# Kernel optimization log

Hardware: AMD Instinct MI355X
Metric: run time of the kernel (lower is better)

The kernel has to match this reference:

```python
import jax, jax.numpy as jnp
import numpy as np

EMBED = 768
HEADS = 12
HEAD_DIM = EMBED // HEADS
HIDDEN = 4 * EMBED
EPS = 1e-5


def setup_inputs() -> dict:
    key = jax.random.key(0)
    ks = jax.random.split(key, 12)
    s = lambda fan_in: 1.0 / np.sqrt(fan_in)
    return {
        "x": jax.random.normal(ks[0], (4, 2048, EMBED), dtype=jnp.float32),
        "ln1_g": jnp.ones((EMBED,), jnp.float32),
        "ln1_b": jnp.zeros((EMBED,), jnp.float32),
        "qkv_w": jax.random.normal(ks[1], (EMBED, 3 * EMBED), jnp.float32) * s(EMBED),
        "qkv_b": jnp.zeros((3 * EMBED,), jnp.float32),
        "proj_w": jax.random.normal(ks[2], (EMBED, EMBED), jnp.float32) * s(EMBED),
        "proj_b": jnp.zeros((EMBED,), jnp.float32),
        "ln2_g": jnp.ones((EMBED,), jnp.float32),
        "ln2_b": jnp.zeros((EMBED,), jnp.float32),
        "fc1_w": jax.random.normal(ks[3], (EMBED, HIDDEN), jnp.float32) * s(EMBED),
        "fc1_b": jnp.zeros((HIDDEN,), jnp.float32),
        "fc2_w": jax.random.normal(ks[4], (HIDDEN, EMBED), jnp.float32) * s(HIDDEN),
        "fc2_b": jnp.zeros((EMBED,), jnp.float32),
    }


def _layernorm(x, g, b):
    mu = jnp.mean(x, axis=-1, keepdims=True)
    var = jnp.var(x, axis=-1, keepdims=True)
    return (x - mu) * jax.lax.rsqrt(var + EPS) * g + b


def reference(x, ln1_g, ln1_b, qkv_w, qkv_b, proj_w, proj_b,
              ln2_g, ln2_b, fc1_w, fc1_b, fc2_w, fc2_b):
    B, N, C = x.shape
    # --- attention (pre-LN) ---
    xn = _layernorm(x, ln1_g, ln1_b)
    qkv = xn @ qkv_w + qkv_b                       # [B,N,3C]
    qkv = qkv.reshape(B, N, 3, HEADS, HEAD_DIM)
    q, k, v = jnp.moveaxis(qkv, 2, 0)              # each [B,N,H,D]
    q = jnp.swapaxes(q, 1, 2)                      # [B,H,N,D]
    k = jnp.swapaxes(k, 1, 2)
    v = jnp.swapaxes(v, 1, 2)
    scale = HEAD_DIM ** -0.5
    attn = jax.nn.softmax(jnp.einsum('bhnd,bhmd->bhnm', q, k) * scale, axis=-1)
    out = jnp.einsum('bhnm,bhmd->bhnd', attn, v)   # [B,H,N,D]
    out = jnp.swapaxes(out, 1, 2).reshape(B, N, C)
    out = out @ proj_w + proj_b
    x = x + out
    # --- MLP (pre-LN) ---
    xn2 = _layernorm(x, ln2_g, ln2_b)
    h = jax.nn.gelu(xn2 @ fc1_w + fc1_b, approximate=False)
    x = x + (h @ fc2_w + fc2_b)
    return x
```

## Files before the change

kernel.cpp:

```cpp
#include <hip/hip_runtime.h>

typedef unsigned short ushort_t;
typedef __attribute__((ext_vector_type(8))) unsigned short ushort8;
typedef __attribute__((ext_vector_type(4))) unsigned short ushort4v;
typedef __attribute__((ext_vector_type(2))) unsigned int uint2v;
typedef __attribute__((ext_vector_type(4))) float f32x4;
typedef __attribute__((ext_vector_type(8))) __bf16 bf16x8;

#define DEVFN static __device__ __forceinline__

DEVFN unsigned short f2bf(float f) {
    unsigned int u = __builtin_bit_cast(unsigned int, f);
    u += 0x7FFFu + ((u >> 16) & 1u);
    return (unsigned short)(u >> 16);
}

DEVFN bf16x8 ldsfrag(const ushort_t* p) {
    ushort8 u = *reinterpret_cast<const ushort8*>(p);
    return __builtin_bit_cast(bf16x8, u);
}

DEVFN bf16x8 ldg8(const ushort_t* p) {
    ushort8 u = *reinterpret_cast<const ushort8*>(p);
    return __builtin_bit_cast(bf16x8, u);
}

DEVFN f32x4 mfma16(bf16x8 a, bf16x8 b, f32x4 c) {
    return __builtin_amdgcn_mfma_f32_16x16x32_bf16(a, b, c, 0, 0, 0);
}

DEVFN void gl2lds16(const ushort_t* g, ushort_t* l) {
    __builtin_amdgcn_global_load_lds(
        (const __attribute__((address_space(1))) unsigned int*)g,
        (__attribute__((address_space(3))) unsigned int*)l, 16, 0, 0);
}

DEVFN unsigned int cvtpk(float lo, float hi) {
    unsigned int r;
    asm("v_cvt_pk_bf16_f32 %0, %1, %2" : "=v"(r) : "v"(lo), "v"(hi));
    return r;
}

DEVFN float gelu_fast(float v) {
    const float a = 0.7978845608f * v * fmaf(0.044715f, v * v, 1.0f);
    const float e = __builtin_amdgcn_exp2f(2.885390082f * a);
    const float th = 1.0f - 2.0f * __builtin_amdgcn_rcpf(e + 1.0f);
    return 0.5f * v * (1.0f + th);
}

__global__ __launch_bounds__(256) void wt4_kernel(
    const float* __restrict__ qkv_w, const float* __restrict__ proj_w,
    const float* __restrict__ fc1_w, const float* __restrict__ fc2_w,
    ushort_t* __restrict__ qkv_wt, ushort_t* __restrict__ proj_wt,
    ushort_t* __restrict__ fc1_wt, ushort_t* __restrict__ fc2_wt) {
    __shared__ float t[32][33];
    const int bid = blockIdx.x;
    const float* in; ushort_t* out; int K, N, n0, k0;
    if (bid < 1728)      { in = qkv_w;  out = qkv_wt;  K = 768;  N = 2304;
                           n0 = (bid % 72) * 32;  k0 = (bid / 72) * 32; }
    else if (bid < 2304) { const int r = bid - 1728; in = proj_w; out = proj_wt;
                           K = 768;  N = 768;
                           n0 = (r % 24) * 32;    k0 = (r / 24) * 32; }
    else if (bid < 4608) { const int r = bid - 2304; in = fc1_w;  out = fc1_wt;
                           K = 768;  N = 3072;
                           n0 = (r % 96) * 32;    k0 = (r / 96) * 32; }
    else                 { const int r = bid - 4608; in = fc2_w;  out = fc2_wt;
                           K = 3072; N = 768;
                           n0 = (r % 24) * 32;    k0 = (r / 24) * 32; }
    const int tx = threadIdx.x & 31, ty = threadIdx.x >> 5;
    for (int j = 0; j < 4; j++)
        t[ty + 8 * j][tx] = in[(size_t)(k0 + ty + 8 * j) * N + n0 + tx];
    __syncthreads();
    for (int j = 0; j < 4; j++)
        out[(size_t)(n0 + ty + 8 * j) * K + k0 + tx] = f2bf(t[tx][ty + 8 * j]);
}

__global__ __launch_bounds__(256) void ln_kernel(const float* __restrict__ x,
                                                 const float* __restrict__ g,
                                                 const float* __restrict__ bta,
                                                 ushort_t* __restrict__ out) {
    const int row = blockIdx.x;
    const int tid = threadIdx.x;
    const float* xr = x + (size_t)row * 768;
    float v0 = xr[tid], v1 = xr[tid + 256], v2 = xr[tid + 512];
    float s = v0 + v1 + v2;
    float q = v0 * v0 + v1 * v1 + v2 * v2;
    for (int d = 32; d; d >>= 1) {
        s += __shfl_down(s, d);
        q += __shfl_down(q, d);
    }
    __shared__ float red[8];
    const int w = tid >> 6, lane = tid & 63;
    if (lane == 0) { red[w] = s; red[4 + w] = q; }
    __syncthreads();
    if (tid == 0) {
        float ts = red[0] + red[1] + red[2] + red[3];
        float tq = red[4] + red[5] + red[6] + red[7];
        float mu = ts * (1.0f / 768.0f);
        float var = tq * (1.0f / 768.0f) - mu * mu;
        red[0] = mu;
        red[1] = rsqrtf(var + 1e-5f);
    }
    __syncthreads();
    const float mu = red[0], rs = red[1];
    ushort_t* orow = out + (size_t)row * 768;
    orow[tid]       = f2bf((v0 - mu) * rs * g[tid]       + bta[tid]);
    orow[tid + 256] = f2bf((v1 - mu) * rs * g[tid + 256] + bta[tid + 256]);
    orow[tid + 512] = f2bf((v2 - mu) * rs * g[tid + 512] + bta[tid + 512]);
}

enum { EPI_QKV = 0, EPI_RES = 1, EPI_GELU = 2 };

template <int EPI, int BN, int BK>
__global__ __launch_bounds__(256) void gemm_kernel(
    const ushort_t* __restrict__ A, const ushort_t* __restrict__ BT,
    const float* __restrict__ bias, const float* __restrict__ resid,
    float* __restrict__ outf, ushort_t* __restrict__ outb,
    ushort_t* __restrict__ vtout, int M, int N, int K) {
    constexpr int NT = BN / 32;
    constexpr int SL = BK / 8;
    constexpr int SM = SL - 1;
    constexpr int RPI = 64 / SL;
    constexpr int AI = 128 / RPI / 4;
    constexpr int BI = BN / RPI / 4;
    __shared__ __align__(16) ushort_t As[2][128 * BK];
    __shared__ __align__(16) ushort_t Bs[2][BN * BK];
    const int bn = blockIdx.x, bm = blockIdx.y;
    const int tid = threadIdx.x;
    const int lane = tid & 63, w = tid >> 6;
    const int wm = (w >> 1) * 64, wn = (w & 1) * (BN / 2);
    const int l15 = lane & 15, l4 = lane >> 4;

    const int srow = lane / SL;
    const int scol = ((lane & SM) ^ (srow & SM)) * 8;
    const ushort_t* gA = A + (size_t)(bm * 128 + w * (AI * RPI) + srow) * K + scol;
    const ushort_t* gB = BT + (size_t)(bn * BN + w * (BI * RPI) + srow) * K + scol;

    const int swm = l15 & SM;
    int aoff[BK / 32], boff[BK / 32];
#pragma unroll
    for (int kk = 0; kk < BK / 32; kk++) {
        aoff[kk] = (wm + l15) * BK + ((((kk << 2) | l4) ^ swm) * 8);
        boff[kk] = (wn + l15) * BK + ((((kk << 2) | l4) ^ swm) * 8);
    }

    f32x4 acc[4][NT] = {};

    auto stage = [&](int k0, int buf) {
#pragma unroll
        for (int i = 0; i < AI; i++)
            gl2lds16(gA + k0 + i * RPI * K, &As[buf][(w * AI + i) * 512]);
#pragma unroll
        for (int i = 0; i < BI; i++)
            gl2lds16(gB + k0 + i * RPI * K, &Bs[buf][(w * BI + i) * 512]);
    };

    stage(0, 0);
    __syncthreads();
    int cur = 0;
    for (int k0 = 0; k0 < K; k0 += BK) {
        if (k0 + BK < K) stage(k0 + BK, cur ^ 1);
#pragma unroll
        for (int kk = 0; kk < BK / 32; kk++) {
            bf16x8 af[4], bfr[NT];
#pragma unroll
            for (int mt = 0; mt < 4; mt++)
                af[mt] = ldsfrag(As[cur] + aoff[kk] + mt * 16 * BK);
#pragma unroll
            for (int nt = 0; nt < NT; nt++)
                bfr[nt] = ldsfrag(Bs[cur] + boff[kk] + nt * 16 * BK);
#pragma unroll
            for (int mt = 0; mt < 4; mt++)
#pragma unroll
                for (int nt = 0; nt < NT; nt++)
                    acc[mt][nt] = mfma16(bfr[nt], af[mt], acc[mt][nt]);
        }
        __syncthreads();
        cur ^= 1;
    }

#pragma unroll
    for (int nt = 0; nt < NT; nt++) {
        const int gc0 = bn * BN + wn + nt * 16 + l4 * 4;
        const f32x4 bi = *reinterpret_cast<const f32x4*>(bias + gc0);
#pragma unroll
        for (int mt = 0; mt < 4; mt++) {
            const int gr = bm * 128 + wm + mt * 16 + l15;
            f32x4 v = acc[mt][nt] + bi;
            if constexpr (EPI == EPI_QKV) {
                if (gc0 < 768) v *= 0.18033688011f;
                if (gc0 >= 1536) {
                    const int d = gc0 - 1536;
                    const int h = d >> 6, dh = d & 63;
                    const int b = gr >> 11, tl = gr & 2047;
                    ushort_t* vrow = vtout + ((size_t)((b * 12 + h) * 64 + dh)) * 2048 + tl;
                    vrow[0]        = f2bf(v[0]);
                    vrow[2048]     = f2bf(v[1]);
                    vrow[2 * 2048] = f2bf(v[2]);
                    vrow[3 * 2048] = f2bf(v[3]);
                } else {
                    uint2v o;
                    o[0] = cvtpk(v[0], v[1]);
                    o[1] = cvtpk(v[2], v[3]);
                    *reinterpret_cast<uint2v*>(outb + (size_t)gr * N + gc0) = o;
                }
            } else if constexpr (EPI == EPI_RES) {
                const f32x4 rsd = *reinterpret_cast<const f32x4*>(resid + (size_t)gr * N + gc0);
                *reinterpret_cast<f32x4*>(outf + (size_t)gr * N + gc0) = v + rsd;
            } else {
                f32x4 gl;
#pragma unroll
                for (int r = 0; r < 4; r++) gl[r] = gelu_fast(v[r]);
                uint2v o;
                o[0] = cvtpk(gl[0], gl[1]);
                o[1] = cvtpk(gl[2], gl[3]);
                *reinterpret_cast<uint2v*>(outb + (size_t)gr * N + gc0) = o;
            }
        }
    }
}

__global__ __launch_bounds__(256, 4) void attn_kernel(const ushort_t* __restrict__ qkv,
                                                      const ushort_t* __restrict__ vt,
                                                      ushort_t* __restrict__ out) {
    __shared__ __align__(16) ushort_t Kb[2][4096];
    __shared__ __align__(16) ushort_t Vb[2][4096];
    __shared__ __align__(16) ushort_t Ps[4][1024];

    const int bid = blockIdx.x;
    const int nid = (bid & 7) * 192 + (bid >> 3);
    const int qt = nid & 31;
    const int bh = nid >> 5;
    const int b = bh / 12, h = bh % 12;
    const int tid = threadIdx.x;
    const int lane = tid & 63, w = tid >> 6;
    const int l15 = lane & 15, l4 = lane >> 4;

    const ushort_t* qrow = qkv + (size_t)(b * 2048 + qt * 64 + w * 16 + l15) * 2304 + h * 64;
    const bf16x8 aq0 = ldg8(qrow + l4 * 8);
    const bf16x8 aq1 = ldg8(qrow + 32 + l4 * 8);

    const int jr0 = w * 16 + (lane >> 3);
    const int jr1 = jr0 + 8;
    const int c0 = ((lane & 7) ^ (jr0 & 7)) * 8;
    const int c1 = ((lane & 7) ^ (jr1 & 7)) * 8;
    const ushort_t* kg0 = qkv + (size_t)(b * 2048 + jr0) * 2304 + 768 + h * 64 + c0;
    const ushort_t* kg1 = qkv + (size_t)(b * 2048 + jr1) * 2304 + 768 + h * 64 + c1;
    const ushort_t* vg0 = vt + (size_t)(bh * 64 + jr0) * 2048 + c0;
    const ushort_t* vg1 = vt + (size_t)(bh * 64 + jr1) * 2048 + c1;

    const int sw7 = l15 & 7;
    const int ka0 = l15 * 64 + ((l4 ^ sw7) * 8);
    const int ka1 = l15 * 64 + (((4 + l4) ^ sw7) * 8);

    ushort_t* const psw = Ps[w];
    const int pw_m = l15 & 14;
    int pwoff[4];
#pragma unroll
    for (int jt = 0; jt < 4; jt++) pwoff[jt] = l15 * 64 + (((jt * 4 + l4) ^ pw_m) * 4);
    const int pr0 = l15 * 64 + (((2 * l4) ^ pw_m) * 4);
    const int pr1 = l15 * 64 + (((8 + 2 * l4) ^ pw_m) * 4);

    float lrun = 0.f;
    f32x4 oacc[4] = {};

    gl2lds16(kg0, &Kb[0][w * 1024]);
    gl2lds16(kg1, &Kb[0][w * 1024 + 512]);
    gl2lds16(vg0, &Vb[0][w * 1024]);
    gl2lds16(vg1, &Vb[0][w * 1024 + 512]);
    __syncthreads();

    for (int kt = 0; kt < 32; kt++) {
        const int cur = kt & 1;
        if (kt < 31) {
            const size_t ko = (size_t)(kt + 1) * 64 * 2304;
            const int vo = (kt + 1) * 64;
            gl2lds16(kg0 + ko, &Kb[cur ^ 1][w * 1024]);
            gl2lds16(kg1 + ko, &Kb[cur ^ 1][w * 1024 + 512]);
            gl2lds16(vg0 + vo, &Vb[cur ^ 1][w * 1024]);
            gl2lds16(vg1 + vo, &Vb[cur ^ 1][w * 1024 + 512]);
        }
        const ushort_t* kb = Kb[cur];
        const ushort_t* vb = Vb[cur];

        f32x4 st[4];
        __builtin_amdgcn_s_setprio(1);
#pragma unroll
        for (int jt = 0; jt < 4; jt++) {
            f32x4 z = {};
            z = mfma16(ldsfrag(kb + ka0 + jt * 1024), aq0, z);
            z = mfma16(ldsfrag(kb + ka1 + jt * 1024), aq1, z);
            st[jt] = z;
        }
        __builtin_amdgcn_s_setprio(0);

        float rs = 0.f;
#pragma unroll
        for (int jt = 0; jt < 4; jt++) {
            const float p0 = __builtin_amdgcn_exp2f(st[jt][0]);
            const float p1 = __builtin_amdgcn_exp2f(st[jt][1]);
            const float p2 = __builtin_amdgcn_exp2f(st[jt][2]);
            const float p3 = __builtin_amdgcn_exp2f(st[jt][3]);
            rs += (p0 + p1) + (p2 + p3);
            uint2v pw;
            pw[0] = cvtpk(p0, p1);
            pw[1] = cvtpk(p2, p3);
            *reinterpret_cast<uint2v*>(psw + pwoff[jt]) = pw;
        }
        lrun += rs;

        const bf16x8 pf0 = ldsfrag(psw + pr0);
        const bf16x8 pf1 = ldsfrag(psw + pr1);

        __builtin_amdgcn_s_setprio(1);
#pragma unroll
        for (int dt = 0; dt < 4; dt++) {
            const bf16x8 vf0 = ldsfrag(vb + ka0 + dt * 1024);
            const bf16x8 vf1 = ldsfrag(vb + ka1 + dt * 1024);
            oacc[dt] = mfma16(vf0, pf0, oacc[dt]);
            oacc[dt] = mfma16(vf1, pf1, oacc[dt]);
        }
        __builtin_amdgcn_s_setprio(0);
        __syncthreads();
    }

    lrun += __shfl_xor(lrun, 16);
    lrun += __shfl_xor(lrun, 32);
    const float linv = __builtin_amdgcn_rcpf(lrun);

    ushort_t* orow = out + (size_t)(b * 2048 + qt * 64 + w * 16 + l15) * 768 + h * 64 + l4 * 4;
#pragma unroll
    for (int dt = 0; dt < 4; dt++) {
        ushort4v o;
#pragma unroll
        for (int r = 0; r < 4; r++) o[r] = f2bf(oacc[dt][r] * linv);
        *reinterpret_cast<ushort4v*>(orow + dt * 16) = o;
    }
}

extern "C" void kernel_launch(void* const* d_in, const int* in_sizes, int n_in,
                              void* d_out, int out_size, void* d_ws, size_t ws_size,
                              hipStream_t stream) {
    const float* x      = (const float*)d_in[0];
    const float* ln1_g  = (const float*)d_in[1];
    const float* ln1_b  = (const float*)d_in[2];
    const float* qkv_w  = (const float*)d_in[3];
    const float* qkv_b  = (const float*)d_in[4];
    const float* proj_w = (const float*)d_in[5];
    const float* proj_b = (const float*)d_in[6];
    const float* ln2_g  = (const float*)d_in[7];
    const float* ln2_b  = (const float*)d_in[8];
    const float* fc1_w  = (const float*)d_in[9];
    const float* fc1_b  = (const float*)d_in[10];
    const float* fc2_w  = (const float*)d_in[11];
    const float* fc2_b  = (const float*)d_in[12];
    float* out = (float*)d_out;

    char* ws = (char*)d_ws;
    ushort_t* qkv_wt  = (ushort_t*)(ws);
    ushort_t* proj_wt = (ushort_t*)(ws + 3538944);
    ushort_t* fc1_wt  = (ushort_t*)(ws + 4718592);
    ushort_t* fc2_wt  = (ushort_t*)(ws + 9437184);
    ushort_t* xb      = (ushort_t*)(ws + 14155776);
    ushort_t* aob     = (ushort_t*)(ws + 26738688);
    ushort_t* qkvb    = (ushort_t*)(ws + 39321600);
    ushort_t* vtb     = (ushort_t*)(ws + 77070336);
    ushort_t* hb      = (ushort_t*)(ws + 39321600);

    dim3 blk(256);

    wt4_kernel<<<dim3(6912), blk, 0, stream>>>(qkv_w, proj_w, fc1_w, fc2_w,
                                               qkv_wt, proj_wt, fc1_wt, fc2_wt);
    ln_kernel<<<8192, blk, 0, stream>>>(x, ln1_g, ln1_b, xb);
    gemm_kernel<EPI_QKV, 128, 32><<<dim3(18, 64), blk, 0, stream>>>(
        xb, qkv_wt, qkv_b, nullptr, nullptr, qkvb, vtb, 8192, 2304, 768);
    attn_kernel<<<dim3(1536), blk, 0, stream>>>(qkvb, vtb, aob);
    gemm_kernel<EPI_RES, 64, 64><<<dim3(12, 64), blk, 0, stream>>>(
        aob, proj_wt, proj_b, x, out, nullptr, nullptr, 8192, 768, 768);
    ln_kernel<<<8192, blk, 0, stream>>>(out, ln2_g, ln2_b, xb);
    gemm_kernel<EPI_GELU, 128, 32><<<dim3(24, 64), blk, 0, stream>>>(
        xb, fc1_wt, fc1_b, nullptr, nullptr, hb, nullptr, 8192, 3072, 768);
    gemm_kernel<EPI_RES, 64, 64><<<dim3(12, 64), blk, 0, stream>>>(
        hb, fc2_wt, fc2_b, out, out, nullptr, nullptr, 8192, 768, 3072);
}
```

Measured before the change: 313.8 us.

## Switch GEMMs to 32x32 MFMA with triple-buffered LDS and register-resident P in attention

The GEMM kernel is rewritten to use 32x32x16 bf16 MFMA tiles with a k-major LDS layout and a three-stage global-to-LDS pipeline that waits on explicit vmcnt instead of a full double-buffer sync. In attention, the P matrix is kept in registers and fed straight into 16x16x16 MFMAs for the PV product, removing the per-warp LDS round trip, and occupancy is raised to 5 blocks. This adds inline asm with hand-placed nops and waitcnt counts, which risks hazards or incorrect ordering if the counts do not match the issued loads.

```diff
diff --git a/kernel.cpp b/kernel.cpp
--- a/kernel.cpp
+++ b/kernel.cpp
@@ -2,9 +2,9 @@
 
 typedef unsigned short ushort_t;
 typedef __attribute__((ext_vector_type(8))) unsigned short ushort8;
-typedef __attribute__((ext_vector_type(4))) unsigned short ushort4v;
 typedef __attribute__((ext_vector_type(2))) unsigned int uint2v;
 typedef __attribute__((ext_vector_type(4))) float f32x4;
+typedef __attribute__((ext_vector_type(16))) float f32x16;
 typedef __attribute__((ext_vector_type(8))) __bf16 bf16x8;
 
 #define DEVFN static __device__ __forceinline__
@@ -20,6 +20,10 @@
     return __builtin_bit_cast(bf16x8, u);
 }
 
+DEVFN uint2v ld64u(const ushort_t* p) {
+    return *reinterpret_cast<const uint2v*>(p);
+}
+
 DEVFN bf16x8 ldg8(const ushort_t* p) {
     ushort8 u = *reinterpret_cast<const ushort8*>(p);
     return __builtin_bit_cast(bf16x8, u);
@@ -27,6 +31,14 @@
 
 DEVFN f32x4 mfma16(bf16x8 a, bf16x8 b, f32x4 c) {
     return __builtin_amdgcn_mfma_f32_16x16x32_bf16(a, b, c, 0, 0, 0);
+}
+
+DEVFN f32x16 mfma32(bf16x8 a, bf16x8 b, f32x16 c) {
+    return __builtin_amdgcn_mfma_f32_32x32x16_bf16(a, b, c, 0, 0, 0);
+}
+
+DEVFN void mfmaPV(uint2v a, uint2v b, f32x4& c) {
+    asm("v_mfma_f32_16x16x16_bf16 %0, %1, %2, %0" : "+v"(c) : "v"(a), "v"(b));
 }
 
 DEVFN void gl2lds16(const ushort_t* g, ushort_t* l) {
@@ -111,121 +123,121 @@
 
 enum { EPI_QKV = 0, EPI_RES = 1, EPI_GELU = 2 };
 
-template <int EPI, int BN, int BK>
+template <int EPI, int BN>
 __global__ __launch_bounds__(256) void gemm_kernel(
     const ushort_t* __restrict__ A, const ushort_t* __restrict__ BT,
     const float* __restrict__ bias, const float* __restrict__ resid,
     float* __restrict__ outf, ushort_t* __restrict__ outb,
     ushort_t* __restrict__ vtout, int M, int N, int K) {
-    constexpr int NT = BN / 32;
-    constexpr int SL = BK / 8;
-    constexpr int SM = SL - 1;
-    constexpr int RPI = 64 / SL;
-    constexpr int AI = 128 / RPI / 4;
-    constexpr int BI = BN / RPI / 4;
-    __shared__ __align__(16) ushort_t As[2][128 * BK];
-    __shared__ __align__(16) ushort_t Bs[2][BN * BK];
+    constexpr int NW = BN / 64;
+    constexpr int BSZ = BN * 32;
+    __shared__ __align__(16) ushort_t AsF[3 * 4096];
+    __shared__ __align__(16) ushort_t BsF[3 * BSZ];
     const int bn = blockIdx.x, bm = blockIdx.y;
     const int tid = threadIdx.x;
     const int lane = tid & 63, w = tid >> 6;
     const int wm = (w >> 1) * 64, wn = (w & 1) * (BN / 2);
-    const int l15 = lane & 15, l4 = lane >> 4;
-
-    const int srow = lane / SL;
-    const int scol = ((lane & SM) ^ (srow & SM)) * 8;
-    const ushort_t* gA = A + (size_t)(bm * 128 + w * (AI * RPI) + srow) * K + scol;
-    const ushort_t* gB = BT + (size_t)(bn * BN + w * (BI * RPI) + srow) * K + scol;
-
-    const int swm = l15 & SM;
-    int aoff[BK / 32], boff[BK / 32];
-#pragma unroll
-    for (int kk = 0; kk < BK / 32; kk++) {
-        aoff[kk] = (wm + l15) * BK + ((((kk << 2) | l4) ^ swm) * 8);
-        boff[kk] = (wn + l15) * BK + ((((kk << 2) | l4) ^ swm) * 8);
-    }
-
-    f32x4 acc[4][NT] = {};
-
-    auto stage = [&](int k0, int buf) {
-#pragma unroll
-        for (int i = 0; i < AI; i++)
-            gl2lds16(gA + k0 + i * RPI * K, &As[buf][(w * AI + i) * 512]);
-#pragma unroll
-        for (int i = 0; i < BI; i++)
-            gl2lds16(gB + k0 + i * RPI * K, &Bs[buf][(w * BI + i) * 512]);
+    const int a31 = lane & 31, hi = lane >> 5;
+
+    const ushort_t* gAw = A + (size_t)(bm * 128 + lane) * K + w * 8;
+    const ushort_t* gBw = BT + (size_t)(bn * BN + lane) * K + w * 8;
+
+    const int xbase = (hi * 128 + wm + a31) * 8;
+    const int wbase = (hi * BN + wn + a31) * 8;
+
+    f32x16 acc[2][NW] = {};
+
+    auto stage = [&](int k0, int c) {
+        gl2lds16(gAw + k0, AsF + c * 4096 + (w * 128) * 8);
+        gl2lds16(gAw + k0 + (size_t)64 * K, AsF + c * 4096 + (w * 128 + 64) * 8);
+        gl2lds16(gBw + k0, BsF + c * BSZ + (w * BN) * 8);
+        if constexpr (BN == 128)
+            gl2lds16(gBw + k0 + (size_t)64 * K, BsF + c * BSZ + (w * BN + 64) * 8);
     };
 
+    const int nk = K / 32;
     stage(0, 0);
-    __syncthreads();
-    int cur = 0;
-    for (int k0 = 0; k0 < K; k0 += BK) {
-        if (k0 + BK < K) stage(k0 + BK, cur ^ 1);
-#pragma unroll
-        for (int kk = 0; kk < BK / 32; kk++) {
-            bf16x8 af[4], bfr[NT];
-#pragma unroll
-            for (int mt = 0; mt < 4; mt++)
-                af[mt] = ldsfrag(As[cur] + aoff[kk] + mt * 16 * BK);
-#pragma unroll
-            for (int nt = 0; nt < NT; nt++)
-                bfr[nt] = ldsfrag(Bs[cur] + boff[kk] + nt * 16 * BK);
-#pragma unroll
-            for (int mt = 0; mt < 4; mt++)
-#pragma unroll
-                for (int nt = 0; nt < NT; nt++)
-                    acc[mt][nt] = mfma16(bfr[nt], af[mt], acc[mt][nt]);
-        }
-        __syncthreads();
-        cur ^= 1;
-    }
-
-#pragma unroll
-    for (int nt = 0; nt < NT; nt++) {
-        const int gc0 = bn * BN + wn + nt * 16 + l4 * 4;
-        const f32x4 bi = *reinterpret_cast<const f32x4*>(bias + gc0);
-#pragma unroll
-        for (int mt = 0; mt < 4; mt++) {
-            const int gr = bm * 128 + wm + mt * 16 + l15;
-            f32x4 v = acc[mt][nt] + bi;
-            if constexpr (EPI == EPI_QKV) {
-                if (gc0 < 768) v *= 0.18033688011f;
-                if (gc0 >= 1536) {
-                    const int d = gc0 - 1536;
-                    const int h = d >> 6, dh = d & 63;
-                    const int b = gr >> 11, tl = gr & 2047;
-                    ushort_t* vrow = vtout + ((size_t)((b * 12 + h) * 64 + dh)) * 2048 + tl;
-                    vrow[0]        = f2bf(v[0]);
-                    vrow[2048]     = f2bf(v[1]);
-                    vrow[2 * 2048] = f2bf(v[2]);
-                    vrow[3 * 2048] = f2bf(v[3]);
+    stage(32, 1);
+    int c0 = 0, c1 = 1, c2 = 2;
+    int k0 = 0;
+    for (int t = 0; t < nk; ++t, k0 += 32) {
+        if (t + 1 < nk) {
+            if constexpr (BN == 128) asm volatile("s_waitcnt vmcnt(4)" ::: "memory");
+            else                     asm volatile("s_waitcnt vmcnt(3)" ::: "memory");
+        } else {
+            asm volatile("s_waitcnt vmcnt(0)" ::: "memory");
+        }
+        __builtin_amdgcn_s_barrier();
+        if (t + 2 < nk) stage(k0 + 64, c2);
+        const ushort_t* Ab = AsF + c0 * 4096;
+        const ushort_t* Bb = BsF + c0 * BSZ;
+#pragma unroll
+        for (int ks = 0; ks < 2; ks++) {
+            bf16x8 wb[NW], xa[2];
+#pragma unroll
+            for (int ni = 0; ni < NW; ni++)
+                wb[ni] = ldsfrag(Bb + wbase + ks * BN * 16 + ni * 256);
+#pragma unroll
+            for (int mi = 0; mi < 2; mi++)
+                xa[mi] = ldsfrag(Ab + xbase + ks * 2048 + mi * 256);
+#pragma unroll
+            for (int mi = 0; mi < 2; mi++)
+#pragma unroll
+                for (int ni = 0; ni < NW; ni++)
+                    acc[mi][ni] = mfma32(wb[ni], xa[mi], acc[mi][ni]);
+        }
+        const int tmp = c0; c0 = c1; c1 = c2; c2 = tmp;
+    }
+
+#pragma unroll
+    for (int ni = 0; ni < NW; ni++) {
+#pragma unroll
+        for (int q = 0; q < 4; q++) {
+            const int nb = bn * BN + wn + ni * 32 + 8 * q + 4 * hi;
+            const f32x4 bi = *reinterpret_cast<const f32x4*>(bias + nb);
+#pragma unroll
+            for (int mi = 0; mi < 2; mi++) {
+                const int m = bm * 128 + wm + mi * 32 + a31;
+                f32x4 v;
+#pragma unroll
+                for (int r = 0; r < 4; r++) v[r] = acc[mi][ni][q * 4 + r];
+                v += bi;
+                if constexpr (EPI == EPI_QKV) {
+                    if (nb < 768) v *= 0.18033688011f;
+                    if (nb >= 1536) {
+                        const int d = nb - 1536;
+                        const int h = d >> 6, dh = d & 63;
+                        const int b = m >> 11, tl = m & 2047;
+                        ushort_t* vrow = vtout + ((size_t)((b * 12 + h) * 64 + dh)) * 2048 + tl;
+                        vrow[0]        = f2bf(v[0]);
+                        vrow[2048]     = f2bf(v[1]);
+                        vrow[2 * 2048] = f2bf(v[2]);
+                        vrow[3 * 2048] = f2bf(v[3]);
+                    } else {
+                        uint2v o;
+                        o[0] = cvtpk(v[0], v[1]);
+                        o[1] = cvtpk(v[2], v[3]);
+                        *reinterpret_cast<uint2v*>(outb + (size_t)m * N + nb) = o;
+                    }
+                } else if constexpr (EPI == EPI_RES) {
+                    const f32x4 rsd = *reinterpret_cast<const f32x4*>(resid + (size_t)m * N + nb);
+                    *reinterpret_cast<f32x4*>(outf + (size_t)m * N + nb) = v + rsd;
                 } else {
                     uint2v o;
-                    o[0] = cvtpk(v[0], v[1]);
-                    o[1] = cvtpk(v[2], v[3]);
-                    *reinterpret_cast<uint2v*>(outb + (size_t)gr * N + gc0) = o;
+                    o[0] = cvtpk(gelu_fast(v[0]), gelu_fast(v[1]));
+                    o[1] = cvtpk(gelu_fast(v[2]), gelu_fast(v[3]));
+                    *reinterpret_cast<uint2v*>(outb + (size_t)m * N + nb) = o;
                 }
-            } else if constexpr (EPI == EPI_RES) {
-                const f32x4 rsd = *reinterpret_cast<const f32x4*>(resid + (size_t)gr * N + gc0);
-                *reinterpret_cast<f32x4*>(outf + (size_t)gr * N + gc0) = v + rsd;
-            } else {
-                f32x4 gl;
-#pragma unroll
-                for (int r = 0; r < 4; r++) gl[r] = gelu_fast(v[r]);
-                uint2v o;
-                o[0] = cvtpk(gl[0], gl[1]);
-                o[1] = cvtpk(gl[2], gl[3]);
-                *reinterpret_cast<uint2v*>(outb + (size_t)gr * N + gc0) = o;
             }
         }
     }
 }
 
-__global__ __launch_bounds__(256, 4) void attn_kernel(const ushort_t* __restrict__ qkv,
+__global__ __launch_bounds__(256, 5) void attn_kernel(const ushort_t* __restrict__ qkv,
                                                       const ushort_t* __restrict__ vt,
                                                       ushort_t* __restrict__ out) {
     __shared__ __align__(16) ushort_t Kb[2][4096];
     __shared__ __align__(16) ushort_t Vb[2][4096];
-    __shared__ __align__(16) ushort_t Ps[4][1024];
 
     const int bid = blockIdx.x;
     const int nid = (bid & 7) * 192 + (bid >> 3);
@@ -252,14 +264,10 @@
     const int sw7 = l15 & 7;
     const int ka0 = l15 * 64 + ((l4 ^ sw7) * 8);
     const int ka1 = l15 * 64 + (((4 + l4) ^ sw7) * 8);
-
-    ushort_t* const psw = Ps[w];
-    const int pw_m = l15 & 14;
-    int pwoff[4];
-#pragma unroll
-    for (int jt = 0; jt < 4; jt++) pwoff[jt] = l15 * 64 + (((jt * 4 + l4) ^ pw_m) * 4);
-    const int pr0 = l15 * 64 + (((2 * l4) ^ pw_m) * 4);
-    const int pr1 = l15 * 64 + (((8 + 2 * l4) ^ pw_m) * 4);
+    int voffj[4];
+#pragma unroll
+    for (int jt = 0; jt < 4; jt++)
+        voffj[jt] = (((jt * 2 + (l4 >> 1)) ^ sw7) * 8) + (l4 & 1) * 4;
 
     float lrun = 0.f;
     f32x4 oacc[4] = {};
@@ -295,6 +303,7 @@
         __builtin_amdgcn_s_setprio(0);
 
         float rs = 0.f;
+        uint2v pk[4];
 #pragma unroll
         for (int jt = 0; jt < 4; jt++) {
             const float p0 = __builtin_amdgcn_exp2f(st[jt][0]);
@@ -302,27 +311,24 @@
             const float p2 = __builtin_amdgcn_exp2f(st[jt][2]);
             const float p3 = __builtin_amdgcn_exp2f(st[jt][3]);
             rs += (p0 + p1) + (p2 + p3);
-            uint2v pw;
-            pw[0] = cvtpk(p0, p1);
-            pw[1] = cvtpk(p2, p3);
-            *reinterpret_cast<uint2v*>(psw + pwoff[jt]) = pw;
+            pk[jt][0] = cvtpk(p0, p1);
+            pk[jt][1] = cvtpk(p2, p3);
         }
         lrun += rs;
 
-        const bf16x8 pf0 = ldsfrag(psw + pr0);
-        const bf16x8 pf1 = ldsfrag(psw + pr1);
-
+        const ushort_t* vrow = vb + l15 * 64;
+        asm volatile("s_nop 1");
         __builtin_amdgcn_s_setprio(1);
 #pragma unroll
-        for (int dt = 0; dt < 4; dt++) {
-            const bf16x8 vf0 = ldsfrag(vb + ka0 + dt * 1024);
-            const bf16x8 vf1 = ldsfrag(vb + ka1 + dt * 1024);
-            oacc[dt] = mfma16(vf0, pf0, oacc[dt]);
-            oacc[dt] = mfma16(vf1, pf1, oacc[dt]);
-        }
+        for (int jt = 0; jt < 4; jt++)
+#pragma unroll
+            for (int dt = 0; dt < 4; dt++)
+                mfmaPV(ld64u(vrow + dt * 1024 + voffj[jt]), pk[jt], oacc[dt]);
         __builtin_amdgcn_s_setprio(0);
         __syncthreads();
     }
+
+    asm volatile("s_nop 7\ns_nop 7");
 
     lrun += __shfl_xor(lrun, 16);
     lrun += __shfl_xor(lrun, 32);
@@ -331,10 +337,10 @@
     ushort_t* orow = out + (size_t)(b * 2048 + qt * 64 + w * 16 + l15) * 768 + h * 64 + l4 * 4;
 #pragma unroll
     for (int dt = 0; dt < 4; dt++) {
-        ushort4v o;
-#pragma unroll
-        for (int r = 0; r < 4; r++) o[r] = f2bf(oacc[dt][r] * linv);
-        *reinterpret_cast<ushort4v*>(orow + dt * 16) = o;
+        uint2v o;
+        o[0] = cvtpk(oacc[dt][0] * linv, oacc[dt][1] * linv);
+        o[1] = cvtpk(oacc[dt][2] * linv, oacc[dt][3] * linv);
+        *reinterpret_cast<uint2v*>(orow + dt * 16) = o;
     }
 }
 
@@ -372,14 +378,14 @@
     wt4_kernel<<<dim3(6912), blk, 0, stream>>>(qkv_w, proj_w, fc1_w, fc2_w,
                                                qkv_wt, proj_wt, fc1_wt, fc2_wt);
     ln_kernel<<<8192, blk, 0, stream>>>(x, ln1_g, ln1_b, xb);
-    gemm_kernel<EPI_QKV, 128, 32><<<dim3(18, 64), blk, 0, stream>>>(
+    gemm_kernel<EPI_QKV, 128><<<dim3(18, 64), blk, 0, stream>>>(
         xb, qkv_wt, qkv_b, nullptr, nullptr, qkvb, vtb, 8192, 2304, 768);
     attn_kernel<<<dim3(1536), blk, 0, stream>>>(qkvb, vtb, aob);
-    gemm_kernel<EPI_RES, 64, 64><<<dim3(12, 64), blk, 0, stream>>>(
+    gemm_kernel<EPI_RES, 64><<<dim3(12, 64), blk, 0, stream>>>(
         aob, proj_wt, proj_b, x, out, nullptr, nullptr, 8192, 768, 768);
     ln_kernel<<<8192, blk, 0, stream>>>(out, ln2_g, ln2_b, xb);
-    gemm_kernel<EPI_GELU, 128, 32><<<dim3(24, 64), blk, 0, stream>>>(
+    gemm_kernel<EPI_GELU, 128><<<dim3(24, 64), blk, 0, stream>>>(
         xb, fc1_wt, fc1_b, nullptr, nullptr, hb, nullptr, 8192, 3072, 768);
-    gemm_kernel<EPI_RES, 64, 64><<<dim3(12, 64), blk, 0, stream>>>(
+    gemm_kernel<EPI_RES, 64><<<dim3(12, 64), blk, 0, stream>>>(
         hb, fc2_wt, fc2_b, out, out, nullptr, nullptr, 8192, 768, 3072);
 }
```

After: 430.3 us. 1.37x slower.
